# Performance work log

Hardware: AMD Instinct MI355X
Metric: run time of the kernel (lower is better)

Reference implementation:

```python
import jax, jax.numpy as jnp
import numpy as np

N, E, D_IN, HD, H = 50000, 800000, 768, 64, 4
HC = HD * H


def _gat(x, src, dst, etypes, lin_w, att_src, att_dst, edge_emb, lin_edge_w, att_edge,
         bias, res_w, res_b, ln_g, ln_b):
    # Faithful PyG GATConv (edge_dim, concat=True, add_self_loops=True with
    # fill_value='mean', negative_slope=0.2) + residual + LayerNorm. Eval mode: no dropout.
    n = x.shape[0]
    h, c = att_src.shape
    xs = (x @ lin_w).reshape(n, h, c)                      # [N,H,C]
    a_src = jnp.einsum('nhc,hc->nh', xs, att_src)          # [N,H]
    a_dst = jnp.einsum('nhc,hc->nh', xs, att_dst)
    eattr = edge_emb[etypes]                               # [E,ed]
    ones = jnp.ones((etypes.shape[0],), x.dtype)
    cnt = jax.ops.segment_sum(ones, dst, num_segments=n)
    # self-loop edge_attr = mean of incoming edge attrs per node (fill_value='mean')
    loop_attr = jax.ops.segment_sum(eattr, dst, num_segments=n) / jnp.maximum(cnt, 1.0)[:, None]
    loop = jnp.arange(n, dtype=src.dtype)
    src_a = jnp.concatenate([src, loop])
    dst_a = jnp.concatenate([dst, loop])
    e_all = jnp.concatenate([eattr, loop_attr], 0)
    a_edge = jnp.einsum('ehc,hc->eh', (e_all @ lin_edge_w).reshape(-1, h, c), att_edge)
    alpha = jax.nn.leaky_relu(a_src[src_a] + a_dst[dst_a] + a_edge, 0.2)   # [Ea,H]
    # edge softmax over incoming edges of each destination node
    amax = jax.ops.segment_max(alpha, dst_a, num_segments=n)
    ea = jnp.exp(alpha - amax[dst_a])
    denom = jax.ops.segment_sum(ea, dst_a, num_segments=n)
    w = ea / (denom[dst_a] + 1e-16)
    out = jax.ops.segment_sum(xs[src_a] * w[:, :, None], dst_a, num_segments=n)
    out = out.reshape(n, h * c) + bias + (x @ res_w + res_b)
    mu = out.mean(-1, keepdims=True)
    var = jnp.mean((out - mu) ** 2, -1, keepdims=True)
    return (out - mu) * jax.lax.rsqrt(var + 1e-5) * ln_g + ln_b


def _forward(features, positions,
             fe_w1, fe_b1, fe_w2, fe_b2, fe_pos_w, fe_pos_b, fe_type_emb, fe_out_w, fe_out_b,
             g1_lin_w, g1_att_src, g1_att_dst, g1_edge_emb, g1_lin_edge_w, g1_att_edge,
             g1_bias, g1_res_w, g1_res_b, g1_ln_g, g1_ln_b,
             g2_lin_w, g2_att_src, g2_att_dst, g2_edge_emb, g2_lin_edge_w, g2_att_edge,
             g2_bias, g2_res_w, g2_res_b, g2_ln_g, g2_ln_b,
             cls_w, cls_b,
             edge_index, aspect_indices, edge_types, node_types):
    # EnhancedFeatureExtractor (eval: dropout = identity)
    hfe = jax.nn.relu(features @ fe_w1 + fe_b1) @ fe_w2 + fe_b2
    hfe = hfe + fe_type_emb[node_types] + positions[:, None] @ fe_pos_w + fe_pos_b
    hfe = hfe @ fe_out_w + fe_out_b
    src, dst = edge_index[0], edge_index[1]
    hid = _gat(hfe, src, dst, edge_types, g1_lin_w, g1_att_src, g1_att_dst, g1_edge_emb,
               g1_lin_edge_w, g1_att_edge, g1_bias, g1_res_w, g1_res_b, g1_ln_g, g1_ln_b)
    hid = jax.nn.relu(hid)
    hid = _gat(hid, src, dst, edge_types, g2_lin_w, g2_att_src, g2_att_dst, g2_edge_emb,
               g2_lin_edge_w, g2_att_edge, g2_bias, g2_res_w, g2_res_b, g2_ln_g, g2_ln_b)
    return hid[aspect_indices] @ cls_w + cls_b


def setup_inputs() -> dict:
    key = jax.random.key(0)
    ks = jax.random.split(key, 40)
    d = {}
    d['features'] = jax.random.normal(ks[0], (N, D_IN), jnp.float32)
    d['edge_index'] = jax.random.randint(ks[1], (2, E), 0, N, jnp.int32)
    d['aspect_indices'] = jax.random.randint(ks[2], (4096,), 0, N, jnp.int32)
    d['edge_types'] = jax.random.randint(ks[3], (E,), 0, 4, jnp.int32)
    d['node_types'] = jax.random.randint(ks[4], (N,), 0, 3, jnp.int32)
    d['positions'] = jax.random.uniform(ks[5], (N,), jnp.float32)

    def rn(i, shape, s=0.05):
        return s * jax.random.normal(ks[i], shape, jnp.float32)

    d['fe_w1'] = rn(6, (D_IN, HD)); d['fe_b1'] = rn(7, (HD,))
    d['fe_w2'] = rn(8, (HD, HD));   d['fe_b2'] = rn(9, (HD,))
    d['fe_pos_w'] = rn(10, (1, HD)); d['fe_pos_b'] = rn(11, (HD,))
    d['fe_type_emb'] = rn(12, (3, HD))
    d['fe_out_w'] = rn(13, (HD, HD)); d['fe_out_b'] = rn(14, (HD,))
    d['g1_lin_w'] = rn(15, (HD, HC))
    d['g1_att_src'] = rn(16, (H, HD)); d['g1_att_dst'] = rn(17, (H, HD))
    d['g1_edge_emb'] = rn(18, (4, 4)); d['g1_lin_edge_w'] = rn(19, (4, HC))
    d['g1_att_edge'] = rn(20, (H, HD))
    d['g1_bias'] = rn(21, (HC,)); d['g1_res_w'] = rn(22, (HD, HC)); d['g1_res_b'] = rn(23, (HC,))
    d['g1_ln_g'] = jnp.ones((HC,), jnp.float32); d['g1_ln_b'] = jnp.zeros((HC,), jnp.float32)
    d['g2_lin_w'] = rn(24, (HC, HD))
    d['g2_att_src'] = rn(25, (1, HD)); d['g2_att_dst'] = rn(26, (1, HD))
    d['g2_edge_emb'] = rn(27, (4, 4)); d['g2_lin_edge_w'] = rn(28, (4, HD))
    d['g2_att_edge'] = rn(29, (1, HD))
    d['g2_bias'] = rn(30, (HD,)); d['g2_res_w'] = rn(31, (HC, HD)); d['g2_res_b'] = rn(32, (HD,))
    d['g2_ln_g'] = jnp.ones((HD,), jnp.float32); d['g2_ln_b'] = jnp.zeros((HD,), jnp.float32)
    d['cls_w'] = rn(33, (HD, 3)); d['cls_b'] = rn(34, (3,))
    return d


def reference(features, edge_index, aspect_indices, edge_types, node_types, positions,
              fe_w1, fe_b1, fe_w2, fe_b2, fe_pos_w, fe_pos_b, fe_type_emb, fe_out_w, fe_out_b,
              g1_lin_w, g1_att_src, g1_att_dst, g1_edge_emb, g1_lin_edge_w, g1_att_edge,
              g1_bias, g1_res_w, g1_res_b, g1_ln_g, g1_ln_b,
              g2_lin_w, g2_att_src, g2_att_dst, g2_edge_emb, g2_lin_edge_w, g2_att_edge,
              g2_bias, g2_res_w, g2_res_b, g2_ln_g, g2_ln_b,
              cls_w, cls_b):
    return _forward(features, positions,
                    fe_w1, fe_b1, fe_w2, fe_b2, fe_pos_w, fe_pos_b, fe_type_emb, fe_out_w, fe_out_b,
                    g1_lin_w, g1_att_src, g1_att_dst, g1_edge_emb, g1_lin_edge_w, g1_att_edge,
                    g1_bias, g1_res_w, g1_res_b, g1_ln_g, g1_ln_b,
                    g2_lin_w, g2_att_src, g2_att_dst, g2_edge_emb, g2_lin_edge_w, g2_att_edge,
                    g2_bias, g2_res_w, g2_res_b, g2_ln_g, g2_ln_b,
                    cls_w, cls_b,
                    edge_index, aspect_indices, edge_types, node_types)
```

## Files before the change

### kernel.cpp

```cpp
#include <hip/hip_runtime.h>


#define LRELU(x) ((x) > 0.f ? (x) : 0.2f * (x))

typedef __attribute__((ext_vector_type(8))) short short8;
typedef __attribute__((ext_vector_type(4))) float floatx4;

__device__ __forceinline__ unsigned short f2bf(float x) {
    union { float f; unsigned int u; } v; v.f = x;
    unsigned int r = (v.u + 0x7FFFu + ((v.u >> 16) & 1u)) >> 16;
    return (unsigned short)r;
}
__device__ __forceinline__ unsigned int cvtpk(float lo, float hi) {
    unsigned int r;
    asm("v_cvt_pk_bf16_f32 %0, %1, %2" : "=v"(r) : "v"(lo), "v"(hi));
    return r;
}
__device__ __forceinline__ float bflo(unsigned int u) {
    return __uint_as_float(u << 16);
}
__device__ __forceinline__ float bfhi(unsigned int u) {
    return __uint_as_float(u & 0xFFFF0000u);
}
__device__ __forceinline__ float bf1(unsigned short u) {
    return __uint_as_float(((unsigned int)u) << 16);
}

__global__ __launch_bounds__(256) void k_front(
    const float* __restrict__ e_emb1, const float* __restrict__ lew1,
    const float* __restrict__ ae1,
    const float* __restrict__ e_emb2, const float* __restrict__ lew2,
    const float* __restrict__ ae2,
    float* __restrict__ aet1, float* __restrict__ aet2,
    const float* __restrict__ w2, const float* __restrict__ outw,
    const float* __restrict__ b2, const float* __restrict__ posb,
    const float* __restrict__ outb, const float* __restrict__ temb,
    const float* __restrict__ posw,
    float* __restrict__ W2p, float* __restrict__ h0,
    float* __restrict__ tadd, float* __restrict__ padd,
    const float* __restrict__ w1, const float* __restrict__ B1,
    const float* __restrict__ B2,
    unsigned short* __restrict__ out_fe1, unsigned short* __restrict__ out_p2)
{
    __shared__ float M1[16];
    __shared__ float M2[4];
    int t = threadIdx.x;
    int b = blockIdx.x;
    if (b == 0) {
        if (t < 16) {
            int d = t >> 2, h = t & 3;
            float s = 0.f;
            for (int c = 0; c < 64; ++c) s += lew1[d * 256 + h * 64 + c] * ae1[h * 64 + c];
            M1[d * 4 + h] = s;
        }
        if (t < 4) {
            float s = 0.f;
            for (int c = 0; c < 64; ++c) s += lew2[t * 64 + c] * ae2[c];
            M2[t] = s;
        }
        __syncthreads();
        if (t < 16) {
            int ty = t >> 2, h = t & 3;
            float s = 0.f;
            for (int d = 0; d < 4; ++d) s += e_emb1[ty * 4 + d] * M1[d * 4 + h];
            aet1[ty * 4 + h] = s;
        }
        if (t < 4) {
            float s = 0.f;
            for (int d = 0; d < 4; ++d) s += e_emb2[t * 4 + d] * M2[d];
            aet2[t] = s;
        }
    } else if (b == 1) {
        int i = t >> 2, jq = (t & 3) * 16;
        float a16[16];
#pragma unroll
        for (int u = 0; u < 16; ++u) a16[u] = 0.f;
        for (int k = 0; k < 64; ++k) {
            float a = w2[i * 64 + k];
            const float* op = outw + k * 64 + jq;
            float4 o0 = *(const float4*)op;
            float4 o1 = *(const float4*)(op + 4);
            float4 o2 = *(const float4*)(op + 8);
            float4 o3 = *(const float4*)(op + 12);
            a16[0] += a * o0.x;  a16[1] += a * o0.y;  a16[2] += a * o0.z;  a16[3] += a * o0.w;
            a16[4] += a * o1.x;  a16[5] += a * o1.y;  a16[6] += a * o1.z;  a16[7] += a * o1.w;
            a16[8] += a * o2.x;  a16[9] += a * o2.y;  a16[10] += a * o2.z; a16[11] += a * o2.w;
            a16[12] += a * o3.x; a16[13] += a * o3.y; a16[14] += a * o3.z; a16[15] += a * o3.w;
        }
#pragma unroll
        for (int u = 0; u < 16; ++u) W2p[i * 64 + jq + u] = a16[u];
        for (int e = t; e < 320; e += 256) {
            int g = e >> 6, j = e & 63;
            float s = 0.f;
            for (int k = 0; k < 64; ++k) {
                float v;
                if (g == 0) v = b2[k] + posb[k];
                else if (g <= 3) v = temb[(g - 1) * 64 + k];
                else v = posw[k];
                s += v * outw[k * 64 + j];
            }
            if (g == 0) h0[j] = s + outb[j];
            else if (g <= 3) tadd[(g - 1) * 64 + j] = s;
            else padd[j] = s;
        }
    } else {
        int idx = (b - 2) * 256 + t;
        if (idx < 768 * 64) {
            int k = idx >> 6, col = idx & 63;
            int c = k >> 6, kl = k & 63, kg = kl >> 3, j = kl & 7;
            out_fe1[((c * 8 + kg) * 64 + col) * 8 + j] = f2bf(w1[k * 64 + col]);
        } else {
            int i2 = idx - 768 * 64;
            int k = i2 >> 7, col = i2 & 127;
            float v = (col < 64) ? B1[k * 64 + col] : B2[k * 64 + col - 64];
            int c = k >> 6, kl = k & 63, kg = kl >> 3, j = kl & 7;
            out_p2[((c * 8 + kg) * 128 + col) * 8 + j] = f2bf(v);
        }
    }
}

__global__ __launch_bounds__(64) void k_fuse2(
    const float* __restrict__ W2p, const float* __restrict__ h0,
    const float* __restrict__ tadd, const float* __restrict__ padd,
    const float* __restrict__ lin_w, const float* __restrict__ res_w,
    const float* __restrict__ bias, const float* __restrict__ res_b,
    unsigned short* __restrict__ bz, float* __restrict__ C0,
    float* __restrict__ T, float* __restrict__ P)
{
    __shared__ float bcol[64];
    int c = blockIdx.x;
    int j = threadIdx.x;
    int cL = c & 255;
    const float* Bsrc = (c < 256) ? lin_w : res_w;
    float bv = Bsrc[j * 256 + cL];
    bcol[j] = bv;
    __syncthreads();
    float s = 0.f;
#pragma unroll 8
    for (int k = 0; k < 64; ++k) s += W2p[j * 64 + k] * bcol[k];
    int kg = j >> 3, jj = j & 7, ct = c >> 7, cl = c & 127;
    bz[((ct * 8 + kg) * 128 + cl) * 8 + jj] = f2bf(s);
    float pc = h0[j] * bv;
    float p0 = tadd[j] * bv, p1 = tadd[64 + j] * bv, p2 = tadd[128 + j] * bv;
    float pp = padd[j] * bv;
#pragma unroll
    for (int k = 32; k; k >>= 1) {
        pc += __shfl_xor(pc, k, 64); p0 += __shfl_xor(p0, k, 64);
        p1 += __shfl_xor(p1, k, 64); p2 += __shfl_xor(p2, k, 64);
        pp += __shfl_xor(pp, k, 64);
    }
    if (j == 0) {
        C0[c] = pc + ((c >= 256) ? (bias[cL] + res_b[cL]) : 0.f);
        T[c] = p0; T[512 + c] = p1; T[1024 + c] = p2;
        P[c] = pp;
    }
}

__global__ __launch_bounds__(256) void k_fe1(
    const float* __restrict__ feat, const unsigned short* __restrict__ bswz,
    const float* __restrict__ b1, unsigned short* __restrict__ t1b, int N)
{
    int t = threadIdx.x;
    int wv = t >> 6, lane = t & 63;
    int quad = lane >> 4, l16 = lane & 15;
    long rw = (long)blockIdx.x * 64 + wv * 16;
    long ra = rw + l16;
    if (ra >= N) ra = N - 1;
    const float* fbase = feat + ra * 768 + quad * 8;

    floatx4 acc[4];
#pragma unroll
    for (int i = 0; i < 4; ++i) acc[i] = (floatx4){0.f, 0.f, 0.f, 0.f};

    for (int ci = 0; ci < 12; ++ci) {
        const float* fc = fbase + ci * 64;
        short8 af[2];
#pragma unroll
        for (int s = 0; s < 2; ++s) {
            float4 x = *(const float4*)(fc + s * 32);
            float4 y = *(const float4*)(fc + s * 32 + 4);
            uint4 u = {cvtpk(x.x, x.y), cvtpk(x.z, x.w),
                       cvtpk(y.x, y.y), cvtpk(y.z, y.w)};
            af[s] = *(short8*)&u;
        }
#pragma unroll
        for (int s = 0; s < 2; ++s) {
            int kg = s * 4 + quad;
#pragma unroll
            for (int ct = 0; ct < 4; ++ct) {
                short8 bfrag = *(const short8*)&bswz[
                    ((ci * 8 + kg) * 64 + ct * 16 + l16) * 8];
                acc[ct] = __builtin_amdgcn_mfma_f32_16x16x32_bf16(
                    af[s], bfrag, acc[ct], 0, 0, 0);
            }
        }
    }
#pragma unroll
    for (int ct = 0; ct < 4; ++ct) {
        float bb = b1[ct * 16 + l16];
#pragma unroll
        for (int r = 0; r < 4; ++r) {
            long m = rw + quad * 4 + r;
            if (m < N)
                t1b[m * 64 + ct * 16 + l16] = f2bf(fmaxf(acc[ct][r] + bb, 0.f));
        }
    }
}

__global__ __launch_bounds__(256) void k_prep1(
    const unsigned short* __restrict__ A, const unsigned short* __restrict__ bswz,
    const float* __restrict__ C0, const float* __restrict__ T,
    const float* __restrict__ P, const int* __restrict__ ntypes,
    const float* __restrict__ pos,
    const float* __restrict__ att_s, const float* __restrict__ att_d,
    unsigned short* __restrict__ xsb, unsigned short* __restrict__ resp,
    float* __restrict__ a_src, float* __restrict__ a_dst, int N)
{
    int t = threadIdx.x;
    int wv = t >> 6, lane = t & 63;
    int quad = lane >> 4, l16 = lane & 15;
    long rw = (long)blockIdx.x * 64 + wv * 16;
    int by = blockIdx.y;
    long ra = rw + l16;
    if (ra >= N) ra = N - 1;
    const unsigned short* abase = A + ra * 64 + quad * 8;

    floatx4 acc[8];
#pragma unroll
    for (int i = 0; i < 8; ++i) acc[i] = (floatx4){0.f, 0.f, 0.f, 0.f};

    short8 af[2];
    af[0] = *(const short8*)(abase);
    af[1] = *(const short8*)(abase + 32);
#pragma unroll
    for (int s = 0; s < 2; ++s) {
        int kg = s * 4 + quad;
#pragma unroll
        for (int c8 = 0; c8 < 8; ++c8) {
            short8 bfrag = *(const short8*)&bswz[
                ((by * 8 + kg) * 128 + c8 * 16 + l16) * 8];
            acc[c8] = __builtin_amdgcn_mfma_f32_16x16x32_bf16(
                af[s], bfrag, acc[c8], 0, 0, 0);
        }
    }
    int nta[4];
    float posa[4];
#pragma unroll
    for (int r = 0; r < 4; ++r) {
        long m = rw + quad * 4 + r;
        if (m < N) { nta[r] = ntypes[m]; posa[r] = pos[m]; }
        else       { nta[r] = 0; posa[r] = 0.f; }
    }
    bool isl = (by < 2);
    int cb = by * 128;
    float ps[2][4] = {{0.f,0.f,0.f,0.f},{0.f,0.f,0.f,0.f}};
    float pd[2][4] = {{0.f,0.f,0.f,0.f},{0.f,0.f,0.f,0.f}};
#pragma unroll
    for (int c8 = 0; c8 < 8; ++c8) {
        int gc = cb + c8 * 16 + l16;
        float c0 = C0[gc], pcf = P[gc];
        float as = 0.f, ad = 0.f;
        if (isl) { as = att_s[gc]; ad = att_d[gc]; }
        int hh = c8 >> 2;
#pragma unroll
        for (int r = 0; r < 4; ++r) {
            long m = rw + quad * 4 + r;
            float val = acc[c8][r] + c0 + T[nta[r] * 512 + gc] + posa[r] * pcf;
            if (m < N) {
                if (isl) xsb[m * 256 + gc] = f2bf(val);
                else     resp[m * 256 + gc - 256] = f2bf(val);
            }
            ps[hh][r] += val * as;
            pd[hh][r] += val * ad;
        }
    }
    if (isl) {
#pragma unroll
        for (int h = 0; h < 2; ++h)
#pragma unroll
            for (int r = 0; r < 4; ++r) {
                float a = ps[h][r], b = pd[h][r];
#pragma unroll
                for (int k = 1; k < 16; k <<= 1) {
                    a += __shfl_xor(a, k, 64);
                    b += __shfl_xor(b, k, 64);
                }
                long m = rw + quad * 4 + r;
                if (l16 == 0 && m < N) {
                    int h4 = by * 2 + h;
                    a_src[m * 4 + h4] = a;
                    a_dst[m * 4 + h4] = b;
                }
            }
    }
}

__global__ __launch_bounds__(256) void k_prep2(
    const unsigned short* __restrict__ A, const unsigned short* __restrict__ bswz,
    const float* __restrict__ bias, const float* __restrict__ res_b,
    const float* __restrict__ att_s, const float* __restrict__ att_d,
    unsigned short* __restrict__ xsb, float* __restrict__ resp,
    float* __restrict__ a_src, float* __restrict__ a_dst, int N)
{
    int t = threadIdx.x;
    int wv = t >> 6, lane = t & 63;
    int quad = lane >> 4, l16 = lane & 15;
    long rw = (long)blockIdx.x * 64 + wv * 16;
    long ra = rw + l16;
    if (ra >= N) ra = N - 1;
    const unsigned short* abase = A + ra * 256 + quad * 8;

    floatx4 acc[8];
#pragma unroll
    for (int i = 0; i < 8; ++i) acc[i] = (floatx4){0.f, 0.f, 0.f, 0.f};

    for (int ci = 0; ci < 4; ++ci) {
        short8 af[2];
        af[0] = *(const short8*)(abase + ci * 64);
        af[1] = *(const short8*)(abase + ci * 64 + 32);
#pragma unroll
        for (int s = 0; s < 2; ++s) {
            int kg = s * 4 + quad;
#pragma unroll
            for (int c8 = 0; c8 < 8; ++c8) {
                short8 bfrag = *(const short8*)&bswz[
                    ((ci * 8 + kg) * 128 + c8 * 16 + l16) * 8];
                acc[c8] = __builtin_amdgcn_mfma_f32_16x16x32_bf16(
                    af[s], bfrag, acc[c8], 0, 0, 0);
            }
        }
    }
    float ps[4] = {0.f,0.f,0.f,0.f}, pd[4] = {0.f,0.f,0.f,0.f};
#pragma unroll
    for (int c8 = 0; c8 < 8; ++c8) {
        int gc = c8 * 16 + l16;
        bool isl = gc < 64;
        float badd = isl ? 0.f : (bias[gc - 64] + res_b[gc - 64]);
        float as = isl ? att_s[gc] : 0.f;
        float ad = isl ? att_d[gc] : 0.f;
#pragma unroll
        for (int r = 0; r < 4; ++r) {
            long m = rw + quad * 4 + r;
            float val = acc[c8][r];
            if (m < N) {
                if (isl) xsb[m * 64 + gc] = f2bf(val);
                else     resp[m * 64 + gc - 64] = val + badd;
            }
            if (isl) { ps[r] += val * as; pd[r] += val * ad; }
        }
    }
#pragma unroll
    for (int r = 0; r < 4; ++r) {
        float a = ps[r], b = pd[r];
#pragma unroll
        for (int k = 1; k < 16; k <<= 1) {
            a += __shfl_xor(a, k, 64);
            b += __shfl_xor(b, k, 64);
        }
        long m = rw + quad * 4 + r;
        if (l16 == 0 && m < N) { a_src[m] = a; a_dst[m] = b; }
    }
}

__global__ __launch_bounds__(256) void k_count(
    const int* __restrict__ dst, const int* __restrict__ et,
    int* __restrict__ cnt_t, int E)
{
    int e = blockIdx.x * 256 + threadIdx.x;
    if (e < E) atomicAdd(&cnt_t[dst[e] * 4 + et[e]], 1);
}

__global__ __launch_bounds__(256) void k_scan1(
    const int* __restrict__ cnt_t, int* __restrict__ row_off,
    int* __restrict__ blk_sums, int N)
{
    __shared__ int s[256];
    int t = threadIdx.x;
    int i = blockIdx.x * 256 + t;
    int v = 0;
    if (i < N) v = cnt_t[4 * i] + cnt_t[4 * i + 1] + cnt_t[4 * i + 2] + cnt_t[4 * i + 3];
    s[t] = v;
    __syncthreads();
    for (int off = 1; off < 256; off <<= 1) {
        int x = 0;
        if (t >= off) x = s[t - off];
        __syncthreads();
        s[t] += x;
        __syncthreads();
    }
    if (i < N) row_off[i] = s[t] - v;
    if (t == 255) blk_sums[blockIdx.x] = s[255];
}

__global__ __launch_bounds__(256) void k_scan3(
    int* __restrict__ row_off, int* __restrict__ cursor,
    const int* __restrict__ blk_sums, int N, int E)
{
    __shared__ int s[256];
    int t = threadIdx.x;
    int bid = blockIdx.x;
    s[t] = (t < bid) ? blk_sums[t] : 0;
    __syncthreads();
    for (int off = 128; off; off >>= 1) {
        if (t < off) s[t] += s[t + off];
        __syncthreads();
    }
    int prev = s[0];
    int i = bid * 256 + t;
    if (i < N) {
        int o = row_off[i] + prev;
        row_off[i] = o;
        cursor[i] = o;
    }
    if (i == 0) row_off[N] = E;
}

__global__ __launch_bounds__(256) void k_scatter(
    const int* __restrict__ src, const int* __restrict__ dst,
    const int* __restrict__ et, int* __restrict__ cursor,
    int* __restrict__ csr_pack,
    const float* __restrict__ a_src, const float* __restrict__ a_dst,
    const float* __restrict__ aet1, float* __restrict__ wbuf, int E)
{
    int e = blockIdx.x * 256 + threadIdx.x;
    if (e < E) {
        int d = dst[e];
        int s = src[e];
        int ty = et[e];
        int pos = atomicAdd(&cursor[d], 1);
        csr_pack[pos] = s | (ty << 28);
        float4 as4 = *(const float4*)&a_src[s * 4];
        float4 ad4 = *(const float4*)&a_dst[d * 4];
        float4 ae = *(const float4*)&aet1[ty * 4];
        float a0 = as4.x + ad4.x + ae.x;
        float a1 = as4.y + ad4.y + ae.y;
        float a2 = as4.z + ad4.z + ae.z;
        float a3 = as4.w + ad4.w + ae.w;
        a0 = LRELU(a0); a1 = LRELU(a1); a2 = LRELU(a2); a3 = LRELU(a3);
        float4 w4 = make_float4(expf(a0), expf(a1), expf(a2), expf(a3));
        *(float4*)&wbuf[(long)pos * 4] = w4;
    }
}

__global__ __launch_bounds__(128) void k_gat1(
    const unsigned short* __restrict__ xs1b, const float* __restrict__ a_src,
    const float* __restrict__ a_dst, const int* __restrict__ row_off,
    const int* __restrict__ csr_pack, const float* __restrict__ wbuf,
    const int* __restrict__ cnt_t, const float* __restrict__ aet1,
    const float* __restrict__ ln_g, const float* __restrict__ ln_b,
    const unsigned short* __restrict__ res, unsigned short* __restrict__ out)
{
    __shared__ __align__(16) float4 ws[2][64];
    __shared__ float2 aetp[2][4];
    __shared__ float red[4];
    int n = blockIdx.x;
    int t = threadIdx.x;
    int w = t >> 6, c = t & 63;
    int lc = c & 15, g = c >> 4;
    int h0 = 2 * w;
    if (t < 8) {
        int w2 = t >> 2, ty = t & 3;
        aetp[w2][ty] = make_float2(aet1[ty * 4 + 2 * w2], aet1[ty * 4 + 2 * w2 + 1]);
    }
    int off = row_off[n], deg = row_off[n + 1] - off;
    float2 a_d = *(const float2*)&a_dst[n * 4 + h0];
    __syncthreads();
    float ael0 = 0.f, ael1 = 0.f;
    int degc = 0;
#pragma unroll
    for (int ty = 0; ty < 4; ++ty) {
        int ct = cnt_t[n * 4 + ty];
        degc += ct;
        float2 ae = aetp[w][ty];
        ael0 += (float)ct * ae.x;
        ael1 += (float)ct * ae.y;
    }
    float inv = (degc > 0) ? 1.f / (float)degc : 1.f;
    float2 a_s_self = *(const float2*)&a_src[n * 4 + h0];
    float al0 = a_s_self.x + a_d.x + ael0 * inv;
    float al1 = a_s_self.y + a_d.y + ael1 * inv;
    al0 = LRELU(al0); al1 = LRELU(al1);
    float wself0 = expf(al0), wself1 = expf(al1);

    int col0 = w * 128 + lc * 8;
    const unsigned short* xrow = xs1b + col0;
    float acc[8];
#pragma unroll
    for (int j = 0; j < 8; ++j) acc[j] = 0.f;
    float dp0 = 0.f, dp1 = 0.f;

    for (int base = 0; base < deg; base += 64) {
        int cnt = min(64, deg - base);
        float w0 = 0.f, w1 = 0.f;
        int s = 0;
        if (c < cnt) {
            int idx = off + base + c;
            int pk = csr_pack[idx];
            s = pk & 0x0FFFFFFF;
            float2 wv = *(const float2*)&wbuf[(long)idx * 4 + 2 * w];
            w0 = wv.x; w1 = wv.y;
        }
        dp0 += w0; dp1 += w1;
        ws[w][c] = make_float4(w0, w1, __int_as_float(s), 0.f);
        int cr = (cnt + 7) & ~7;
        for (int i = 0; i < cr; i += 8) {
#pragma unroll
            for (int u = 0; u < 2; ++u) {
                float4 p = ws[w][i + u * 4 + g];
                float wl = (lc < 8) ? p.x : p.y;
                uint4 q = *(const uint4*)&xrow[(long)__float_as_int(p.z) * 256];
                acc[0] += wl * bflo(q.x); acc[1] += wl * bfhi(q.x);
                acc[2] += wl * bflo(q.y); acc[3] += wl * bfhi(q.y);
                acc[4] += wl * bflo(q.z); acc[5] += wl * bfhi(q.z);
                acc[6] += wl * bflo(q.w); acc[7] += wl * bfhi(q.w);
            }
        }
    }
#pragma unroll
    for (int k = 32; k; k >>= 1) {
        dp0 += __shfl_xor(dp0, k, 64);
        dp1 += __shfl_xor(dp1, k, 64);
    }
#pragma unroll
    for (int j = 0; j < 8; ++j) {
        acc[j] += __shfl_xor(acc[j], 16, 64);
        acc[j] += __shfl_xor(acc[j], 32, 64);
    }
    uint4 us = *(const uint4*)&xrow[(long)n * 256];
    float wself_l = (lc < 8) ? wself0 : wself1;
    acc[0] += wself_l * bflo(us.x); acc[1] += wself_l * bfhi(us.x);
    acc[2] += wself_l * bflo(us.y); acc[3] += wself_l * bfhi(us.y);
    acc[4] += wself_l * bflo(us.z); acc[5] += wself_l * bfhi(us.z);
    acc[6] += wself_l * bflo(us.w); acc[7] += wself_l * bfhi(us.w);
    float dsum = ((lc < 8) ? dp0 + wself0 : dp1 + wself1) + 1e-16f;
    float rd = 1.f / dsum;
    uint4 ur = *(const uint4*)&res[(long)n * 256 + col0];
    float v[8];
    v[0] = acc[0] * rd + bflo(ur.x); v[1] = acc[1] * rd + bfhi(ur.x);
    v[2] = acc[2] * rd + bflo(ur.y); v[3] = acc[3] * rd + bfhi(ur.y);
    v[4] = acc[4] * rd + bflo(ur.z); v[5] = acc[5] * rd + bfhi(ur.z);
    v[6] = acc[6] * rd + bflo(ur.w); v[7] = acc[7] * rd + bfhi(ur.w);
    float s1 = 0.f, s2 = 0.f;
#pragma unroll
    for (int j = 0; j < 8; ++j) { s1 += v[j]; s2 += v[j] * v[j]; }
#pragma unroll
    for (int k = 32; k; k >>= 1) {
        s1 += __shfl_xor(s1, k, 64);
        s2 += __shfl_xor(s2, k, 64);
    }
    if (c == 0) { red[w] = s1 * 0.25f; red[2 + w] = s2 * 0.25f; }
    __syncthreads();
    float mu = (red[0] + red[1]) * (1.f / 256.f);
    float var = (red[2] + red[3]) * (1.f / 256.f) - mu * mu;
    float rs = rsqrtf(var + 1e-5f);
    if (g == 0) {
        float4 lg0 = *(const float4*)&ln_g[col0];
        float4 lg1 = *(const float4*)&ln_g[col0 + 4];
        float4 lb0 = *(const float4*)&ln_b[col0];
        float4 lb1 = *(const float4*)&ln_b[col0 + 4];
        float y[8];
        y[0] = fmaxf((v[0] - mu) * rs * lg0.x + lb0.x, 0.f);
        y[1] = fmaxf((v[1] - mu) * rs * lg0.y + lb0.y, 0.f);
        y[2] = fmaxf((v[2] - mu) * rs * lg0.z + lb0.z, 0.f);
        y[3] = fmaxf((v[3] - mu) * rs * lg0.w + lb0.w, 0.f);
        y[4] = fmaxf((v[4] - mu) * rs * lg1.x + lb1.x, 0.f);
        y[5] = fmaxf((v[5] - mu) * rs * lg1.y + lb1.y, 0.f);
        y[6] = fmaxf((v[6] - mu) * rs * lg1.z + lb1.z, 0.f);
        y[7] = fmaxf((v[7] - mu) * rs * lg1.w + lb1.w, 0.f);
        uint4 o;
        o.x = cvtpk(y[0], y[1]); o.y = cvtpk(y[2], y[3]);
        o.z = cvtpk(y[4], y[5]); o.w = cvtpk(y[6], y[7]);
        *(uint4*)&out[(long)n * 256 + col0] = o;
    }
}

__global__ __launch_bounds__(128) void k_gat2(
    const unsigned short* __restrict__ xs2b, const float* __restrict__ a_src,
    const float* __restrict__ a_dst, const int* __restrict__ row_off,
    const int* __restrict__ csr_pack,
    const int* __restrict__ cnt_t, const float* __restrict__ aet2,
    const float* __restrict__ ln_g, const float* __restrict__ ln_b,
    float* io, int N)
{
    __shared__ __align__(8) float2 ws[2][64];
    int v_ = threadIdx.x >> 6, c = threadIdx.x & 63;
    int n = blockIdx.x * 2 + v_;
    if (n >= N) return;
    int lc = c & 15, g = c >> 4;
    int off = row_off[n], deg = row_off[n + 1] - off;
    float a_d = a_dst[n];
    float ael = 0.f;
    int degc = 0;
#pragma unroll
    for (int ty = 0; ty < 4; ++ty) {
        int ct = cnt_t[n * 4 + ty];
        degc += ct;
        ael += (float)ct * aet2[ty];
    }
    ael *= (degc > 0 ? 1.f / (float)degc : 1.f);
    float al = a_src[n] + a_d + ael;
    al = LRELU(al);
    float wself = expf(al);

    int colb = lc * 4;
    const unsigned short* xrow = xs2b + colb;
    float acc[4] = {0.f, 0.f, 0.f, 0.f};
    float dp = 0.f;
    for (int base = 0; base < deg; base += 64) {
        int cnt = min(64, deg - base);
        float we = 0.f;
        int s = 0;
        if (c < cnt) {
            int pk = csr_pack[off + base + c];
            s = pk & 0x0FFFFFFF;
            int ty = ((unsigned)pk) >> 28;
            float a = a_src[s] + a_d + aet2[ty];
            a = LRELU(a);
            we = expf(a);
        }
        dp += we;
        ws[v_][c] = make_float2(we, __int_as_float(s));
        int cr = (cnt + 7) & ~7;
        for (int i = 0; i < cr; i += 8) {
#pragma unroll
            for (int u = 0; u < 2; ++u) {
                float2 p = ws[v_][i + u * 4 + g];
                uint2 q = *(const uint2*)&xrow[(long)__float_as_int(p.y) * 64];
                acc[0] += p.x * bflo(q.x); acc[1] += p.x * bfhi(q.x);
                acc[2] += p.x * bflo(q.y); acc[3] += p.x * bfhi(q.y);
            }
        }
    }
#pragma unroll
    for (int k = 32; k; k >>= 1) dp += __shfl_xor(dp, k, 64);
#pragma unroll
    for (int j = 0; j < 4; ++j) {
        acc[j] += __shfl_xor(acc[j], 16, 64);
        acc[j] += __shfl_xor(acc[j], 32, 64);
    }
    uint2 us = *(const uint2*)&xrow[(long)n * 64];
    acc[0] += wself * bflo(us.x); acc[1] += wself * bfhi(us.x);
    acc[2] += wself * bflo(us.y); acc[3] += wself * bfhi(us.y);
    float dsum = dp + wself + 1e-16f;
    float rd = 1.f / dsum;
    float4 r = *(const float4*)&io[(long)n * 64 + colb];
    float v[4];
    v[0] = acc[0] * rd + r.x; v[1] = acc[1] * rd + r.y;
    v[2] = acc[2] * rd + r.z; v[3] = acc[3] * rd + r.w;
    float s1 = v[0] + v[1] + v[2] + v[3];
    float s2 = v[0] * v[0] + v[1] * v[1] + v[2] * v[2] + v[3] * v[3];
#pragma unroll
    for (int k = 32; k; k >>= 1) {
        s1 += __shfl_xor(s1, k, 64);
        s2 += __shfl_xor(s2, k, 64);
    }
    float mu = s1 * (1.f / 256.f);
    float var = s2 * (1.f / 256.f) - mu * mu;
    float rs = rsqrtf(var + 1e-5f);
    if (g == 0) {
        float4 lg = *(const float4*)&ln_g[colb];
        float4 lb = *(const float4*)&ln_b[colb];
        float4 y;
        y.x = (v[0] - mu) * rs * lg.x + lb.x;
        y.y = (v[1] - mu) * rs * lg.y + lb.y;
        y.z = (v[2] - mu) * rs * lg.z + lb.z;
        y.w = (v[3] - mu) * rs * lg.w + lb.w;
        *(float4*)&io[(long)n * 64 + colb] = y;
    }
}

__global__ __launch_bounds__(256) void k_cls(
    const float* __restrict__ hid2, const int* __restrict__ asp,
    const float* __restrict__ w, const float* __restrict__ b,
    float* __restrict__ out)
{
    int g = blockIdx.x * 256 + threadIdx.x;
    int i = g / 3, j = g - i * 3;
    int a = asp[i];
    float acc = b[j];
#pragma unroll 8
    for (int cc = 0; cc < 64; ++cc) acc += hid2[(long)a * 64 + cc] * w[cc * 3 + j];
    out[i * 3 + j] = acc;
}

extern "C" void kernel_launch(void* const* d_in, const int* in_sizes, int n_in,
                              void* d_out, int out_size, void* d_ws, size_t ws_size,
                              hipStream_t stream)
{
    const float* features    = (const float*)d_in[0];
    const int*   edge_index  = (const int*)d_in[1];
    const int*   aspect      = (const int*)d_in[2];
    const int*   etypes      = (const int*)d_in[3];
    const int*   ntypes      = (const int*)d_in[4];
    const float* pos         = (const float*)d_in[5];
    const float* fe_w1       = (const float*)d_in[6];
    const float* fe_b1       = (const float*)d_in[7];
    const float* fe_w2       = (const float*)d_in[8];
    const float* fe_b2       = (const float*)d_in[9];
    const float* fe_pos_w    = (const float*)d_in[10];
    const float* fe_pos_b    = (const float*)d_in[11];
    const float* fe_type_emb = (const float*)d_in[12];
    const float* fe_out_w    = (const float*)d_in[13];
    const float* fe_out_b    = (const float*)d_in[14];
    const float* g1_lin_w    = (const float*)d_in[15];
    const float* g1_att_src  = (const float*)d_in[16];
    const float* g1_att_dst  = (const float*)d_in[17];
    const float* g1_edge_emb = (const float*)d_in[18];
    const float* g1_lin_edge = (const float*)d_in[19];
    const float* g1_att_edge = (const float*)d_in[20];
    const float* g1_bias     = (const float*)d_in[21];
    const float* g1_res_w    = (const float*)d_in[22];
    const float* g1_res_b    = (const float*)d_in[23];
    const float* g1_ln_g     = (const float*)d_in[24];
    const float* g1_ln_b     = (const float*)d_in[25];
    const float* g2_lin_w    = (const float*)d_in[26];
    const float* g2_att_src  = (const float*)d_in[27];
    const float* g2_att_dst  = (const float*)d_in[28];
    const float* g2_edge_emb = (const float*)d_in[29];
    const float* g2_lin_edge = (const float*)d_in[30];
    const float* g2_att_edge = (const float*)d_in[31];
    const float* g2_bias     = (const float*)d_in[32];
    const float* g2_res_w    = (const float*)d_in[33];
    const float* g2_res_b    = (const float*)d_in[34];
    const float* g2_ln_g     = (const float*)d_in[35];
    const float* g2_ln_b     = (const float*)d_in[36];
    const float* cls_w       = (const float*)d_in[37];
    const float* cls_b       = (const float*)d_in[38];

    const int N = in_sizes[0] / 768;
    const int E = in_sizes[1] / 2;
    const int* src = edge_index;
    const int* dst = edge_index + E;

    char* wsb = (char*)d_ws;
    size_t off = 0;
    auto alloc = [&](size_t bytes) -> char* {
        char* p = wsb + off;
        off += (bytes + 255) & ~(size_t)255;
        return p;
    };
    unsigned short* t1b  = (unsigned short*)alloc((size_t)N * 64 * 2);
    unsigned short* xs1b = (unsigned short*)alloc((size_t)N * 256 * 2);
    unsigned short* xs2b = (unsigned short*)alloc((size_t)N * 64 * 2);
    unsigned short* hid1b= (unsigned short*)alloc((size_t)N * 256 * 2);
    unsigned short* rp1  = (unsigned short*)alloc((size_t)N * 256 * 2);
    float* rp2     = (float*)alloc((size_t)N * 64 * 4);
    float* a_src1  = (float*)alloc((size_t)N * 4 * 4);
    float* a_dst1  = (float*)alloc((size_t)N * 4 * 4);
    float* a_src2  = (float*)alloc((size_t)N * 4);
    float* a_dst2  = (float*)alloc((size_t)N * 4);
    int*   cnt_t   = (int*)alloc((size_t)N * 4 * 4);
    int*   row_off = (int*)alloc((size_t)(N + 1) * 4);
    int*   cursor  = (int*)alloc((size_t)N * 4);
    int*   blk     = (int*)alloc(1024);
    int*   csr_pack= (int*)alloc((size_t)E * 4);
    float* wbuf    = (float*)alloc((size_t)E * 4 * 4);
    float* aet1    = (float*)alloc(64);
    float* aet2    = (float*)alloc(64);
    unsigned short* bz_fe1 = (unsigned short*)alloc(768 * 64 * 2);
    unsigned short* bz_p1  = (unsigned short*)alloc(64 * 512 * 2);
    unsigned short* bz_p2  = (unsigned short*)alloc(256 * 128 * 2);
    float* W2p     = (float*)alloc(64 * 64 * 4);
    float* h0v     = (float*)alloc(64 * 4);
    float* taddv   = (float*)alloc(192 * 4);
    float* paddv   = (float*)alloc(64 * 4);
    float* C0t     = (float*)alloc(512 * 4);
    float* Tt      = (float*)alloc(3 * 512 * 4);
    float* Pt      = (float*)alloc(512 * 4);

    hipMemsetAsync(cnt_t, 0, (size_t)N * 4 * 4, stream);

    int mb = (N + 63) / 64;
    int eblk = (E + 255) / 256;
    int nb = (N + 255) / 256;

    k_front<<<322, 256, 0, stream>>>(
        g1_edge_emb, g1_lin_edge, g1_att_edge,
        g2_edge_emb, g2_lin_edge, g2_att_edge, aet1, aet2,
        fe_w2, fe_out_w, fe_b2, fe_pos_b, fe_out_b, fe_type_emb, fe_pos_w,
        W2p, h0v, taddv, paddv,
        fe_w1, g2_lin_w, g2_res_w, bz_fe1, bz_p2);
    k_fuse2<<<512, 64, 0, stream>>>(W2p, h0v, taddv, paddv, g1_lin_w, g1_res_w,
                                    g1_bias, g1_res_b, bz_p1, C0t, Tt, Pt);
    k_count<<<eblk, 256, 0, stream>>>(dst, etypes, cnt_t, E);
    k_scan1<<<nb, 256, 0, stream>>>(cnt_t, row_off, blk, N);
    k_scan3<<<nb, 256, 0, stream>>>(row_off, cursor, blk, N, E);
    k_fe1<<<mb, 256, 0, stream>>>(features, bz_fe1, fe_b1, t1b, N);
    k_prep1<<<dim3(mb, 4), 256, 0, stream>>>(
        t1b, bz_p1, C0t, Tt, Pt, ntypes, pos, g1_att_src, g1_att_dst,
        xs1b, rp1, a_src1, a_dst1, N);
    k_scatter<<<eblk, 256, 0, stream>>>(src, dst, etypes, cursor, csr_pack,
                                        a_src1, a_dst1, aet1, wbuf, E);
    k_gat1<<<N, 128, 0, stream>>>(xs1b, a_src1, a_dst1, row_off, csr_pack, wbuf,
                                  cnt_t, aet1, g1_ln_g, g1_ln_b, rp1, hid1b);
    k_prep2<<<mb, 256, 0, stream>>>(hid1b, bz_p2, g2_bias, g2_res_b,
                                    g2_att_src, g2_att_dst, xs2b, rp2,
                                    a_src2, a_dst2, N);
    k_gat2<<<(N + 1) / 2, 128, 0, stream>>>(xs2b, a_src2, a_dst2, row_off,
                                            csr_pack, cnt_t, aet2,
                                            g2_ln_g, g2_ln_b, rp2, N);
    k_cls<<<(out_size + 255) / 256, 256, 0, stream>>>(rp2, aspect, cls_w, cls_b,
                                                      (float*)d_out);
}
```

Baseline: 605.0 us.

## Fuse feature-encoder GEMM into GAT1 projection and merge setup kernels

The first feature GEMM (768->64, ReLU) and the layer-1 projection GEMM are merged into one kernel. The 64-wide hidden tile now stays in shared memory instead of going through a global t1b buffer, and each block computes all four column groups in a loop rather than using a 4-wide grid. The weight-folding kernels (W2p and fuse2) are rewritten into k_front using reassociated matrix-vector products, and the edge-count atomics move into the same launch as a grid-stride section. Together these remove several launches and a global round trip, at the cost of less grid parallelism in the fused projection.

```diff
diff --git a/kernel.cpp b/kernel.cpp
--- a/kernel.cpp
+++ b/kernel.cpp
@@ -32,21 +32,25 @@
     const float* __restrict__ e_emb2, const float* __restrict__ lew2,
     const float* __restrict__ ae2,
     float* __restrict__ aet1, float* __restrict__ aet2,
+    const float* __restrict__ w1, const float* __restrict__ B1,
+    const float* __restrict__ B2,
+    unsigned short* __restrict__ out_fe1, unsigned short* __restrict__ out_p2,
     const float* __restrict__ w2, const float* __restrict__ outw,
     const float* __restrict__ b2, const float* __restrict__ posb,
     const float* __restrict__ outb, const float* __restrict__ temb,
     const float* __restrict__ posw,
-    float* __restrict__ W2p, float* __restrict__ h0,
-    float* __restrict__ tadd, float* __restrict__ padd,
-    const float* __restrict__ w1, const float* __restrict__ B1,
-    const float* __restrict__ B2,
-    unsigned short* __restrict__ out_fe1, unsigned short* __restrict__ out_p2)
-{
-    __shared__ float M1[16];
-    __shared__ float M2[4];
+    const float* __restrict__ lin_w, const float* __restrict__ res_w,
+    const float* __restrict__ bias, const float* __restrict__ res_b,
+    unsigned short* __restrict__ bz, float* __restrict__ C0,
+    float* __restrict__ T, float* __restrict__ P,
+    const int* __restrict__ dst, const int* __restrict__ et,
+    int* __restrict__ cnt_t, int E)
+{
     int t = threadIdx.x;
     int b = blockIdx.x;
     if (b == 0) {
+        __shared__ float M1[16];
+        __shared__ float M2[4];
         if (t < 16) {
             int d = t >> 2, h = t & 3;
             float s = 0.f;
@@ -70,41 +74,8 @@
             for (int d = 0; d < 4; ++d) s += e_emb2[t * 4 + d] * M2[d];
             aet2[t] = s;
         }
-    } else if (b == 1) {
-        int i = t >> 2, jq = (t & 3) * 16;
-        float a16[16];
-#pragma unroll
-        for (int u = 0; u < 16; ++u) a16[u] = 0.f;
-        for (int k = 0; k < 64; ++k) {
-            float a = w2[i * 64 + k];
-            const float* op = outw + k * 64 + jq;
-            float4 o0 = *(const float4*)op;
-            float4 o1 = *(const float4*)(op + 4);
-            float4 o2 = *(const float4*)(op + 8);
-            float4 o3 = *(const float4*)(op + 12);
-            a16[0] += a * o0.x;  a16[1] += a * o0.y;  a16[2] += a * o0.z;  a16[3] += a * o0.w;
-            a16[4] += a * o1.x;  a16[5] += a * o1.y;  a16[6] += a * o1.z;  a16[7] += a * o1.w;
-            a16[8] += a * o2.x;  a16[9] += a * o2.y;  a16[10] += a * o2.z; a16[11] += a * o2.w;
-            a16[12] += a * o3.x; a16[13] += a * o3.y; a16[14] += a * o3.z; a16[15] += a * o3.w;
-        }
-#pragma unroll
-        for (int u = 0; u < 16; ++u) W2p[i * 64 + jq + u] = a16[u];
-        for (int e = t; e < 320; e += 256) {
-            int g = e >> 6, j = e & 63;
-            float s = 0.f;
-            for (int k = 0; k < 64; ++k) {
-                float v;
-                if (g == 0) v = b2[k] + posb[k];
-                else if (g <= 3) v = temb[(g - 1) * 64 + k];
-                else v = posw[k];
-                s += v * outw[k * 64 + j];
-            }
-            if (g == 0) h0[j] = s + outb[j];
-            else if (g <= 3) tadd[(g - 1) * 64 + j] = s;
-            else padd[j] = s;
-        }
-    } else {
-        int idx = (b - 2) * 256 + t;
+    } else if (b <= 320) {
+        int idx = (b - 1) * 256 + t;
         if (idx < 768 * 64) {
             int k = idx >> 6, col = idx & 63;
             int c = k >> 6, kl = k & 63, kg = kl >> 3, j = kl & 7;
@@ -116,99 +87,50 @@
             int c = k >> 6, kl = k & 63, kg = kl >> 3, j = kl & 7;
             out_p2[((c * 8 + kg) * 128 + col) * 8 + j] = f2bf(v);
         }
-    }
-}
-
-__global__ __launch_bounds__(64) void k_fuse2(
-    const float* __restrict__ W2p, const float* __restrict__ h0,
-    const float* __restrict__ tadd, const float* __restrict__ padd,
-    const float* __restrict__ lin_w, const float* __restrict__ res_w,
-    const float* __restrict__ bias, const float* __restrict__ res_b,
-    unsigned short* __restrict__ bz, float* __restrict__ C0,
-    float* __restrict__ T, float* __restrict__ P)
-{
-    __shared__ float bcol[64];
-    int c = blockIdx.x;
-    int j = threadIdx.x;
-    int cL = c & 255;
-    const float* Bsrc = (c < 256) ? lin_w : res_w;
-    float bv = Bsrc[j * 256 + cL];
-    bcol[j] = bv;
-    __syncthreads();
-    float s = 0.f;
+    } else if (b <= 448) {
+        __shared__ float sb[4][64];
+        __shared__ float sy[4][64];
+        int wv = t >> 6, j = t & 63;
+        int c = (b - 321) * 4 + wv;
+        int cL = c & 255;
+        const float* Bsrc = (c < 256) ? lin_w : res_w;
+        float bv = Bsrc[j * 256 + cL];
+        sb[wv][j] = bv;
+        __syncthreads();
+        float yj = 0.f;
 #pragma unroll 8
-    for (int k = 0; k < 64; ++k) s += W2p[j * 64 + k] * bcol[k];
-    int kg = j >> 3, jj = j & 7, ct = c >> 7, cl = c & 127;
-    bz[((ct * 8 + kg) * 128 + cl) * 8 + jj] = f2bf(s);
-    float pc = h0[j] * bv;
-    float p0 = tadd[j] * bv, p1 = tadd[64 + j] * bv, p2 = tadd[128 + j] * bv;
-    float pp = padd[j] * bv;
-#pragma unroll
-    for (int k = 32; k; k >>= 1) {
-        pc += __shfl_xor(pc, k, 64); p0 += __shfl_xor(p0, k, 64);
-        p1 += __shfl_xor(p1, k, 64); p2 += __shfl_xor(p2, k, 64);
-        pp += __shfl_xor(pp, k, 64);
-    }
-    if (j == 0) {
-        C0[c] = pc + ((c >= 256) ? (bias[cL] + res_b[cL]) : 0.f);
-        T[c] = p0; T[512 + c] = p1; T[1024 + c] = p2;
-        P[c] = pp;
-    }
-}
-
-__global__ __launch_bounds__(256) void k_fe1(
-    const float* __restrict__ feat, const unsigned short* __restrict__ bswz,
-    const float* __restrict__ b1, unsigned short* __restrict__ t1b, int N)
-{
-    int t = threadIdx.x;
-    int wv = t >> 6, lane = t & 63;
-    int quad = lane >> 4, l16 = lane & 15;
-    long rw = (long)blockIdx.x * 64 + wv * 16;
-    long ra = rw + l16;
-    if (ra >= N) ra = N - 1;
-    const float* fbase = feat + ra * 768 + quad * 8;
-
-    floatx4 acc[4];
-#pragma unroll
-    for (int i = 0; i < 4; ++i) acc[i] = (floatx4){0.f, 0.f, 0.f, 0.f};
-
-    for (int ci = 0; ci < 12; ++ci) {
-        const float* fc = fbase + ci * 64;
-        short8 af[2];
-#pragma unroll
-        for (int s = 0; s < 2; ++s) {
-            float4 x = *(const float4*)(fc + s * 32);
-            float4 y = *(const float4*)(fc + s * 32 + 4);
-            uint4 u = {cvtpk(x.x, x.y), cvtpk(x.z, x.w),
-                       cvtpk(y.x, y.y), cvtpk(y.z, y.w)};
-            af[s] = *(short8*)&u;
-        }
-#pragma unroll
-        for (int s = 0; s < 2; ++s) {
-            int kg = s * 4 + quad;
-#pragma unroll
-            for (int ct = 0; ct < 4; ++ct) {
-                short8 bfrag = *(const short8*)&bswz[
-                    ((ci * 8 + kg) * 64 + ct * 16 + l16) * 8];
-                acc[ct] = __builtin_amdgcn_mfma_f32_16x16x32_bf16(
-                    af[s], bfrag, acc[ct], 0, 0, 0);
-            }
-        }
-    }
-#pragma unroll
-    for (int ct = 0; ct < 4; ++ct) {
-        float bb = b1[ct * 16 + l16];
-#pragma unroll
-        for (int r = 0; r < 4; ++r) {
-            long m = rw + quad * 4 + r;
-            if (m < N)
-                t1b[m * 64 + ct * 16 + l16] = f2bf(fmaxf(acc[ct][r] + bb, 0.f));
-        }
-    }
-}
-
-__global__ __launch_bounds__(256) void k_prep1(
-    const unsigned short* __restrict__ A, const unsigned short* __restrict__ bswz,
+        for (int k = 0; k < 64; ++k) yj += outw[j * 64 + k] * sb[wv][k];
+        sy[wv][j] = yj;
+        __syncthreads();
+        float s = 0.f;
+#pragma unroll 8
+        for (int m = 0; m < 64; ++m) s += w2[j * 64 + m] * sy[wv][m];
+        int kg = j >> 3, jj = j & 7, ct = c >> 7, cl = c & 127;
+        bz[((ct * 8 + kg) * 128 + cl) * 8 + jj] = f2bf(s);
+        float pc = outb[j] * bv + (b2[j] + posb[j]) * yj;
+        float p0 = temb[j] * yj, p1 = temb[64 + j] * yj, p2 = temb[128 + j] * yj;
+        float pp = posw[j] * yj;
+#pragma unroll
+        for (int k = 32; k; k >>= 1) {
+            pc += __shfl_xor(pc, k, 64); p0 += __shfl_xor(p0, k, 64);
+            p1 += __shfl_xor(p1, k, 64); p2 += __shfl_xor(p2, k, 64);
+            pp += __shfl_xor(pp, k, 64);
+        }
+        if (j == 0) {
+            C0[c] = pc + ((c >= 256) ? (bias[cL] + res_b[cL]) : 0.f);
+            T[c] = p0; T[512 + c] = p1; T[1024 + c] = p2;
+            P[c] = pp;
+        }
+    } else {
+        for (int e = (b - 449) * 256 + t; e < E; e += 256 * 256)
+            atomicAdd(&cnt_t[dst[e] * 4 + et[e]], 1);
+    }
+}
+
+__global__ __launch_bounds__(256) void k_fp1(
+    const float* __restrict__ feat, const unsigned short* __restrict__ bzfe,
+    const float* __restrict__ b1,
+    const unsigned short* __restrict__ bzp1,
     const float* __restrict__ C0, const float* __restrict__ T,
     const float* __restrict__ P, const int* __restrict__ ntypes,
     const float* __restrict__ pos,
@@ -216,82 +138,124 @@
     unsigned short* __restrict__ xsb, unsigned short* __restrict__ resp,
     float* __restrict__ a_src, float* __restrict__ a_dst, int N)
 {
+    __shared__ __align__(16) unsigned short tl[64 * 72];
     int t = threadIdx.x;
     int wv = t >> 6, lane = t & 63;
     int quad = lane >> 4, l16 = lane & 15;
-    long rw = (long)blockIdx.x * 64 + wv * 16;
-    int by = blockIdx.y;
-    long ra = rw + l16;
-    if (ra >= N) ra = N - 1;
-    const unsigned short* abase = A + ra * 64 + quad * 8;
-
-    floatx4 acc[8];
-#pragma unroll
-    for (int i = 0; i < 8; ++i) acc[i] = (floatx4){0.f, 0.f, 0.f, 0.f};
-
-    short8 af[2];
-    af[0] = *(const short8*)(abase);
-    af[1] = *(const short8*)(abase + 32);
-#pragma unroll
-    for (int s = 0; s < 2; ++s) {
-        int kg = s * 4 + quad;
-#pragma unroll
-        for (int c8 = 0; c8 < 8; ++c8) {
-            short8 bfrag = *(const short8*)&bswz[
-                ((by * 8 + kg) * 128 + c8 * 16 + l16) * 8];
-            acc[c8] = __builtin_amdgcn_mfma_f32_16x16x32_bf16(
-                af[s], bfrag, acc[c8], 0, 0, 0);
-        }
-    }
+    long rb = (long)blockIdx.x * 64;
+
+    {
+        long ra = rb + wv * 16 + l16;
+        if (ra >= N) ra = N - 1;
+        const float* fbase = feat + ra * 768 + quad * 8;
+        floatx4 acc[4];
+#pragma unroll
+        for (int i = 0; i < 4; ++i) acc[i] = (floatx4){0.f, 0.f, 0.f, 0.f};
+        for (int ci = 0; ci < 12; ++ci) {
+            const float* fc = fbase + ci * 64;
+            short8 af[2];
+#pragma unroll
+            for (int s = 0; s < 2; ++s) {
+                float4 x = *(const float4*)(fc + s * 32);
+                float4 y = *(const float4*)(fc + s * 32 + 4);
+                uint4 u = {cvtpk(x.x, x.y), cvtpk(x.z, x.w),
+                           cvtpk(y.x, y.y), cvtpk(y.z, y.w)};
+                af[s] = *(short8*)&u;
+            }
+#pragma unroll
+            for (int s = 0; s < 2; ++s) {
+                int kg = s * 4 + quad;
+#pragma unroll
+                for (int ct = 0; ct < 4; ++ct) {
+                    short8 bfrag = *(const short8*)&bzfe[
+                        ((ci * 8 + kg) * 64 + ct * 16 + l16) * 8];
+                    acc[ct] = __builtin_amdgcn_mfma_f32_16x16x32_bf16(
+                        af[s], bfrag, acc[ct], 0, 0, 0);
+                }
+            }
+        }
+#pragma unroll
+        for (int ct = 0; ct < 4; ++ct) {
+            float bb = b1[ct * 16 + l16];
+#pragma unroll
+            for (int r = 0; r < 4; ++r) {
+                int row = wv * 16 + quad * 4 + r;
+                tl[row * 72 + ct * 16 + l16] = f2bf(fmaxf(acc[ct][r] + bb, 0.f));
+            }
+        }
+    }
+    __syncthreads();
+
+    int rowB = wv * 16 + l16;
+    short8 af0 = *(const short8*)&tl[rowB * 72 + quad * 8];
+    short8 af1 = *(const short8*)&tl[rowB * 72 + quad * 8 + 32];
+    long rwB = rb + wv * 16;
     int nta[4];
     float posa[4];
 #pragma unroll
     for (int r = 0; r < 4; ++r) {
-        long m = rw + quad * 4 + r;
+        long m = rwB + quad * 4 + r;
         if (m < N) { nta[r] = ntypes[m]; posa[r] = pos[m]; }
         else       { nta[r] = 0; posa[r] = 0.f; }
     }
-    bool isl = (by < 2);
-    int cb = by * 128;
-    float ps[2][4] = {{0.f,0.f,0.f,0.f},{0.f,0.f,0.f,0.f}};
-    float pd[2][4] = {{0.f,0.f,0.f,0.f},{0.f,0.f,0.f,0.f}};
-#pragma unroll
-    for (int c8 = 0; c8 < 8; ++c8) {
-        int gc = cb + c8 * 16 + l16;
-        float c0 = C0[gc], pcf = P[gc];
-        float as = 0.f, ad = 0.f;
-        if (isl) { as = att_s[gc]; ad = att_d[gc]; }
-        int hh = c8 >> 2;
-#pragma unroll
-        for (int r = 0; r < 4; ++r) {
-            long m = rw + quad * 4 + r;
-            float val = acc[c8][r] + c0 + T[nta[r] * 512 + gc] + posa[r] * pcf;
-            if (m < N) {
-                if (isl) xsb[m * 256 + gc] = f2bf(val);
-                else     resp[m * 256 + gc - 256] = f2bf(val);
-            }
-            ps[hh][r] += val * as;
-            pd[hh][r] += val * ad;
-        }
-    }
-    if (isl) {
-#pragma unroll
-        for (int h = 0; h < 2; ++h)
+    for (int by = 0; by < 4; ++by) {
+        floatx4 acc[8];
+#pragma unroll
+        for (int i = 0; i < 8; ++i) acc[i] = (floatx4){0.f, 0.f, 0.f, 0.f};
+#pragma unroll
+        for (int s = 0; s < 2; ++s) {
+            int kg = s * 4 + quad;
+            short8 af = s ? af1 : af0;
+#pragma unroll
+            for (int c8 = 0; c8 < 8; ++c8) {
+                short8 bfrag = *(const short8*)&bzp1[
+                    ((by * 8 + kg) * 128 + c8 * 16 + l16) * 8];
+                acc[c8] = __builtin_amdgcn_mfma_f32_16x16x32_bf16(
+                    af, bfrag, acc[c8], 0, 0, 0);
+            }
+        }
+        bool isl = (by < 2);
+        int cb = by * 128;
+        float ps[2][4] = {{0.f,0.f,0.f,0.f},{0.f,0.f,0.f,0.f}};
+        float pd[2][4] = {{0.f,0.f,0.f,0.f},{0.f,0.f,0.f,0.f}};
+#pragma unroll
+        for (int c8 = 0; c8 < 8; ++c8) {
+            int gc = cb + c8 * 16 + l16;
+            float c0 = C0[gc], pcf = P[gc];
+            float as = 0.f, ad = 0.f;
+            if (isl) { as = att_s[gc]; ad = att_d[gc]; }
+            int hh = c8 >> 2;
 #pragma unroll
             for (int r = 0; r < 4; ++r) {
-                float a = ps[h][r], b = pd[h][r];
-#pragma unroll
-                for (int k = 1; k < 16; k <<= 1) {
-                    a += __shfl_xor(a, k, 64);
-                    b += __shfl_xor(b, k, 64);
+                long m = rwB + quad * 4 + r;
+                float val = acc[c8][r] + c0 + T[nta[r] * 512 + gc] + posa[r] * pcf;
+                if (m < N) {
+                    if (isl) xsb[m * 256 + gc] = f2bf(val);
+                    else     resp[m * 256 + gc - 256] = f2bf(val);
                 }
-                long m = rw + quad * 4 + r;
-                if (l16 == 0 && m < N) {
-                    int h4 = by * 2 + h;
-                    a_src[m * 4 + h4] = a;
-                    a_dst[m * 4 + h4] = b;
+                ps[hh][r] += val * as;
+                pd[hh][r] += val * ad;
+            }
+        }
+        if (isl) {
+#pragma unroll
+            for (int h = 0; h < 2; ++h)
+#pragma unroll
+                for (int r = 0; r < 4; ++r) {
+                    float a = ps[h][r], bq = pd[h][r];
+#pragma unroll
+                    for (int k = 1; k < 16; k <<= 1) {
+                        a += __shfl_xor(a, k, 64);
+                        bq += __shfl_xor(bq, k, 64);
+                    }
+                    long m = rwB + quad * 4 + r;
+                    if (l16 == 0 && m < N) {
+                        int h4 = by * 2 + h;
+                        a_src[m * 4 + h4] = a;
+                        a_dst[m * 4 + h4] = bq;
+                    }
                 }
-            }
+        }
     }
 }
 
@@ -360,14 +324,6 @@
         long m = rw + quad * 4 + r;
         if (l16 == 0 && m < N) { a_src[m] = a; a_dst[m] = b; }
     }
-}
-
-__global__ __launch_bounds__(256) void k_count(
-    const int* __restrict__ dst, const int* __restrict__ et,
-    int* __restrict__ cnt_t, int E)
-{
-    int e = blockIdx.x * 256 + threadIdx.x;
-    if (e < E) atomicAdd(&cnt_t[dst[e] * 4 + et[e]], 1);
 }
 
 __global__ __launch_bounds__(256) void k_scan1(
@@ -739,7 +695,6 @@
         off += (bytes + 255) & ~(size_t)255;
         return p;
     };
-    unsigned short* t1b  = (unsigned short*)alloc((size_t)N * 64 * 2);
     unsigned short* xs1b = (unsigned short*)alloc((size_t)N * 256 * 2);
     unsigned short* xs2b = (unsigned short*)alloc((size_t)N * 64 * 2);
     unsigned short* hid1b= (unsigned short*)alloc((size_t)N * 256 * 2);
@@ -760,10 +715,6 @@
     unsigned short* bz_fe1 = (unsigned short*)alloc(768 * 64 * 2);
     unsigned short* bz_p1  = (unsigned short*)alloc(64 * 512 * 2);
     unsigned short* bz_p2  = (unsigned short*)alloc(256 * 128 * 2);
-    float* W2p     = (float*)alloc(64 * 64 * 4);
-    float* h0v     = (float*)alloc(64 * 4);
-    float* taddv   = (float*)alloc(192 * 4);
-    float* paddv   = (float*)alloc(64 * 4);
     float* C0t     = (float*)alloc(512 * 4);
     float* Tt      = (float*)alloc(3 * 512 * 4);
     float* Pt      = (float*)alloc(512 * 4);
@@ -774,21 +725,18 @@
     int eblk = (E + 255) / 256;
     int nb = (N + 255) / 256;
 
-    k_front<<<322, 256, 0, stream>>>(
+    k_front<<<705, 256, 0, stream>>>(
         g1_edge_emb, g1_lin_edge, g1_att_edge,
         g2_edge_emb, g2_lin_edge, g2_att_edge, aet1, aet2,
+        fe_w1, g2_lin_w, g2_res_w, bz_fe1, bz_p2,
         fe_w2, fe_out_w, fe_b2, fe_pos_b, fe_out_b, fe_type_emb, fe_pos_w,
-        W2p, h0v, taddv, paddv,
-        fe_w1, g2_lin_w, g2_res_w, bz_fe1, bz_p2);
-    k_fuse2<<<512, 64, 0, stream>>>(W2p, h0v, taddv, paddv, g1_lin_w, g1_res_w,
-                                    g1_bias, g1_res_b, bz_p1, C0t, Tt, Pt);
-    k_count<<<eblk, 256, 0, stream>>>(dst, etypes, cnt_t, E);
+        g1_lin_w, g1_res_w, g1_bias, g1_res_b, bz_p1, C0t, Tt, Pt,
+        dst, etypes, cnt_t, E);
     k_scan1<<<nb, 256, 0, stream>>>(cnt_t, row_off, blk, N);
     k_scan3<<<nb, 256, 0, stream>>>(row_off, cursor, blk, N, E);
-    k_fe1<<<mb, 256, 0, stream>>>(features, bz_fe1, fe_b1, t1b, N);
-    k_prep1<<<dim3(mb, 4), 256, 0, stream>>>(
-        t1b, bz_p1, C0t, Tt, Pt, ntypes, pos, g1_att_src, g1_att_dst,
-        xs1b, rp1, a_src1, a_dst1, N);
+    k_fp1<<<mb, 256, 0, stream>>>(
+        features, bz_fe1, fe_b1, bz_p1, C0t, Tt, Pt, ntypes, pos,
+        g1_att_src, g1_att_dst, xs1b, rp1, a_src1, a_dst1, N);
     k_scatter<<<eblk, 256, 0, stream>>>(src, dst, etypes, cursor, csr_pack,
                                         a_src1, a_dst1, aet1, wbuf, E);
     k_gat1<<<N, 128, 0, stream>>>(xs1b, a_src1, a_dst1, row_off, csr_pack, wbuf,
```

Measured after the change: 593.0 us. 1.02x faster.
